# Kernel optimization log

Hardware: AMD Instinct MI355X
Metric: run time of the kernel (lower is better)

Reference implementation:

```python
import jax, jax.numpy as jnp
import numpy as np

N_NODES = 100000
N_EDGES = 1250000
D_FEAT = 64
K = 10          # propagation steps (hardcoded in module)
ALPHA = 0.1     # teleport probability (hardcoded in module)


def setup_inputs() -> dict:
    key = jax.random.key(0)
    k1, k2 = jax.random.split(key)
    x = jax.random.normal(k1, (N_NODES, D_FEAT), dtype=jnp.float32)
    # edge_index[0] = source nodes (j), edge_index[1] = target nodes (i)
    edge_index = jax.random.randint(k2, (2, N_EDGES), 0, N_NODES, dtype=jnp.int32)
    return {"x": x, "edge_index": edge_index}


def reference(x, edge_index):
    # PyG APPNP with add_self_loops=False, dropout=0:
    #   gcn_norm: deg[i] = sum of unit edge weights into i (scatter on col)
    #   norm_e = deg^{-1/2}[row_e] * deg^{-1/2}[col_e]
    #   h_{k+1} = (1 - alpha) * A_hat h_k + alpha * x
    row, col = edge_index[0], edge_index[1]
    ones = jnp.ones((edge_index.shape[1],), dtype=x.dtype)
    deg = jax.ops.segment_sum(ones, col, num_segments=N_NODES)
    dinv_sqrt = jnp.where(deg > 0, jax.lax.rsqrt(jnp.where(deg > 0, deg, 1.0)), 0.0)
    norm = dinv_sqrt[row] * dinv_sqrt[col]  # [E]

    h = x
    for _ in range(K):
        # gather-scale-scatter: messages norm_e * h[src_e], aggregated at dst_e
        msg = norm[:, None] * h[row]                           # [E, D]
        agg = jax.ops.segment_sum(msg, col, num_segments=N_NODES)  # [N, D]
        h = (1.0 - ALPHA) * agg + ALPHA * x
    return h
```

## Files before the change

### kernel.cpp

```cpp
#include <hip/hip_runtime.h>

constexpr int DFEAT  = 64;
constexpr int KSTEPS = 10;
constexpr float ALPHA = 0.1f;
constexpr int PAD    = 4;
constexpr int BSHIFT = 8;
constexpr int MAXBUCK = 512;
constexpr int GR_A   = 128;

constexpr int SCAN_T    = 256;
constexpr int SCAN_I    = 4;
constexpr int SCAN_TILE = SCAN_T * SCAN_I;

typedef unsigned int u32;
typedef __attribute__((ext_vector_type(4))) unsigned int u32x4;

__device__ inline u32 f2bf(float f) {
    u32 u = __float_as_uint(f);
    return ((u + 0x7fffu + ((u >> 16) & 1u)) >> 16) & 0xFFFFu;
}
__device__ inline float bfLO(u32 v) { return __uint_as_float(v << 16); }
__device__ inline float bfHI(u32 v) { return __uint_as_float(v & 0xFFFF0000u); }

__global__ void __launch_bounds__(256) k_hA(
    const int* __restrict__ col, int* __restrict__ blockhist,
    int E, int nb, int chunk) {
    __shared__ int hist[MAXBUCK];
    int t  = threadIdx.x;
    int e0 = blockIdx.x * chunk;
    int e1 = min(E, e0 + chunk);
    for (int b = t; b < MAXBUCK; b += 256) hist[b] = 0;
    __syncthreads();
    for (int e = e0 + t; e < e1; e += 256)
        atomicAdd(&hist[col[e] >> BSHIFT], 1);
    __syncthreads();
    for (int b = t; b < nb; b += 256)
        blockhist[blockIdx.x * MAXBUCK + b] = hist[b];
}

__global__ void k_colsum(int* __restrict__ blockhist, int* __restrict__ btotal) {
    __shared__ int s[GR_A];
    int b = blockIdx.x, t = threadIdx.x;
    int v = blockhist[t * MAXBUCK + b];
    s[t] = v;
    __syncthreads();
    for (int o = 1; o < GR_A; o <<= 1) {
        int u = (t >= o) ? s[t - o] : 0;
        __syncthreads();
        s[t] += u;
        __syncthreads();
    }
    blockhist[t * MAXBUCK + b] = s[t] - v;
    if (t == GR_A - 1) btotal[b] = s[t];
}

__global__ void k_bscan(const int* __restrict__ btotal, int* __restrict__ bstart,
                        int nb) {
    __shared__ int s[MAXBUCK];
    int t = threadIdx.x;
    if (t < nb) s[t] = btotal[t];
    __syncthreads();
    if (t == 0) {
        int acc = 0;
        for (int i = 0; i < nb; ++i) { int v = s[i]; s[i] = acc; acc += v; }
    }
    __syncthreads();
    if (t < nb) bstart[t] = s[t];
}

__global__ void __launch_bounds__(256) k_hB(
    const int* __restrict__ row, const int* __restrict__ col,
    const int* __restrict__ blockhist, const int* __restrict__ bstart,
    u32* __restrict__ bucketed, int E, int nb, int chunk) {
    __shared__ int cur[MAXBUCK];
    int t  = threadIdx.x;
    int e0 = blockIdx.x * chunk;
    int e1 = min(E, e0 + chunk);
    for (int b = t; b < nb; b += 256)
        cur[b] = bstart[b] + blockhist[blockIdx.x * MAXBUCK + b];
    __syncthreads();
    for (int e = e0 + t; e < e1; e += 256) {
        int c = col[e], r = row[e];
        int rank = atomicAdd(&cur[c >> BSHIFT], 1);
        bucketed[rank] = ((u32)r << BSHIFT) | (u32)(c & ((1 << BSHIFT) - 1));
    }
}

__global__ void __launch_bounds__(256) k_degB(
    const u32* __restrict__ bucketed, const int* __restrict__ bstart,
    const int* __restrict__ btotal, float* __restrict__ dinv,
    int* __restrict__ dpad, int N) {
    __shared__ int cnt[256];
    int b = blockIdx.x, t = threadIdx.x;
    cnt[t] = 0;
    __syncthreads();
    int p0 = bstart[b], p1 = p0 + btotal[b];
    for (int p = p0 + t; p < p1; p += 256)
        atomicAdd(&cnt[bucketed[p] & 255u], 1);
    __syncthreads();
    int node = (b << BSHIFT) + t;
    if (node < N) {
        int d = cnt[t];
        dinv[node] = (d > 0) ? rsqrtf((float)d) : 0.0f;
        dpad[node] = (d + (PAD - 1)) & ~(PAD - 1);
    }
}

__global__ void k_scan1(const int* __restrict__ in, int* __restrict__ out,
                        int* __restrict__ bsum, int n) {
    __shared__ int s[SCAN_T];
    int tid  = threadIdx.x;
    int base = blockIdx.x * SCAN_TILE + tid * SCAN_I;
    int v[SCAN_I];
    int sum = 0;
#pragma unroll
    for (int j = 0; j < SCAN_I; ++j) {
        v[j] = (base + j < n) ? in[base + j] : 0;
        sum += v[j];
    }
    s[tid] = sum;
    __syncthreads();
    for (int ofs = 1; ofs < SCAN_T; ofs <<= 1) {
        int t = (tid >= ofs) ? s[tid - ofs] : 0;
        __syncthreads();
        s[tid] += t;
        __syncthreads();
    }
    int excl = (tid == 0) ? 0 : s[tid - 1];
    if (tid == SCAN_T - 1) bsum[blockIdx.x] = s[tid];
#pragma unroll
    for (int j = 0; j < SCAN_I; ++j) {
        if (base + j < n) out[base + j] = excl;
        excl += v[j];
    }
}

__global__ void k_scan2(int* __restrict__ bsum, int nb) {
    if (threadIdx.x == 0 && blockIdx.x == 0) {
        int acc = 0;
        for (int i = 0; i < nb; ++i) { int t = bsum[i]; bsum[i] = acc; acc += t; }
    }
}

__global__ void k_scan3(int* __restrict__ offs, const int* __restrict__ bsum, int n) {
    int add  = bsum[blockIdx.x];
    int base = blockIdx.x * SCAN_TILE + threadIdx.x * SCAN_I;
#pragma unroll
    for (int j = 0; j < SCAN_I; ++j) {
        int i = base + j;
        if (i < n) offs[i] += add;
    }
}

__global__ void __launch_bounds__(256) k_fillB(
    const u32* __restrict__ bucketed, const int* __restrict__ bstart,
    const int* __restrict__ btotal, const int* __restrict__ offs,
    const float* __restrict__ dinv, u32* __restrict__ meta, int N) {
    __shared__ int   lcur[256];
    __shared__ float ldinv[256];
    int b = blockIdx.x, t = threadIdx.x;
    int node = (b << BSHIFT) + t;
    lcur[t]  = (node < N) ? offs[node] : 0;
    ldinv[t] = (node < N) ? dinv[node] : 0.0f;
    __syncthreads();
    int p0 = bstart[b], p1 = p0 + btotal[b];
    for (int p = p0 + t; p < p1; p += 256) {
        u32 v  = bucketed[p];
        int r  = (int)(v >> BSHIFT);
        int cl = (int)(v & 255u);
        int pos = atomicAdd(&lcur[cl], 1);
        float w = dinv[r] * ldinv[cl];
        u32 wq = (u32)__float2int_rn(w * 32768.0f);
        if (wq > 32767u) wq = 32767u;
        meta[pos] = (wq << 17) | (u32)r;
    }
}

__global__ void k_cvt(const float* __restrict__ x, u32* __restrict__ xb, int n8) {
    int stride = gridDim.x * blockDim.x;
    const float4* x4 = (const float4*)x;
    u32x4* o4 = (u32x4*)xb;
    for (int i = blockIdx.x * blockDim.x + threadIdx.x; i < n8; i += stride) {
        float4 a = x4[2 * i], b = x4[2 * i + 1];
        u32x4 o;
        o.x = (f2bf(a.y) << 16) | f2bf(a.x);
        o.y = (f2bf(a.w) << 16) | f2bf(a.z);
        o.z = (f2bf(b.y) << 16) | f2bf(b.x);
        o.w = (f2bf(b.w) << 16) | f2bf(b.z);
        o4[i] = o;
    }
}

template<bool LAST>
__global__ void __launch_bounds__(256) k_prop(
    const int* __restrict__ offs, const int* __restrict__ dpad,
    const u32* __restrict__ meta, const u32* __restrict__ hsrc,
    const float* __restrict__ x, const u32* __restrict__ xb,
    void* __restrict__ hdst, int N) {
    int gid = (int)((blockIdx.x * blockDim.x + threadIdx.x) >> 3);
    int l   = threadIdx.x & 7;
    if (gid >= N) return;
    int j   = offs[gid];
    int end = j + dpad[gid];

    const u32x4* h4 = (const u32x4*)hsrc;
    float a0 = 0.f, a1 = 0.f, a2 = 0.f, a3 = 0.f,
          a4 = 0.f, a5 = 0.f, a6 = 0.f, a7 = 0.f;

    if (j < end) {
        u32x4 mq = *(const u32x4*)&meta[j];
        while (j < end) {
            int jn = j + 4;
            u32x4 mqn = *(const u32x4*)&meta[jn];
            u32x4 q0 = h4[(size_t)(mq.x & 0x1FFFFu) * 8 + l];
            u32x4 q1 = h4[(size_t)(mq.y & 0x1FFFFu) * 8 + l];
            u32x4 q2 = h4[(size_t)(mq.z & 0x1FFFFu) * 8 + l];
            u32x4 q3 = h4[(size_t)(mq.w & 0x1FFFFu) * 8 + l];
            float w0 = (float)(mq.x >> 17) * (1.0f / 32768.0f);
            float w1 = (float)(mq.y >> 17) * (1.0f / 32768.0f);
            float w2 = (float)(mq.z >> 17) * (1.0f / 32768.0f);
            float w3 = (float)(mq.w >> 17) * (1.0f / 32768.0f);
            a0 += w0 * bfLO(q0.x); a1 += w0 * bfHI(q0.x);
            a2 += w0 * bfLO(q0.y); a3 += w0 * bfHI(q0.y);
            a4 += w0 * bfLO(q0.z); a5 += w0 * bfHI(q0.z);
            a6 += w0 * bfLO(q0.w); a7 += w0 * bfHI(q0.w);
            a0 += w1 * bfLO(q1.x); a1 += w1 * bfHI(q1.x);
            a2 += w1 * bfLO(q1.y); a3 += w1 * bfHI(q1.y);
            a4 += w1 * bfLO(q1.z); a5 += w1 * bfHI(q1.z);
            a6 += w1 * bfLO(q1.w); a7 += w1 * bfHI(q1.w);
            a0 += w2 * bfLO(q2.x); a1 += w2 * bfHI(q2.x);
            a2 += w2 * bfLO(q2.y); a3 += w2 * bfHI(q2.y);
            a4 += w2 * bfLO(q2.z); a5 += w2 * bfHI(q2.z);
            a6 += w2 * bfLO(q2.w); a7 += w2 * bfHI(q2.w);
            a0 += w3 * bfLO(q3.x); a1 += w3 * bfHI(q3.x);
            a2 += w3 * bfLO(q3.y); a3 += w3 * bfHI(q3.y);
            a4 += w3 * bfLO(q3.z); a5 += w3 * bfHI(q3.z);
            a6 += w3 * bfLO(q3.w); a7 += w3 * bfHI(q3.w);
            mq = mqn; j = jn;
        }
    }

    if (LAST) {
        size_t base = (size_t)gid * DFEAT + (size_t)l * 8;
        float4 xa = *(const float4*)&x[base];
        float4 xc = *(const float4*)&x[base + 4];
        float r0 = (1.0f - ALPHA) * a0 + ALPHA * xa.x;
        float r1 = (1.0f - ALPHA) * a1 + ALPHA * xa.y;
        float r2 = (1.0f - ALPHA) * a2 + ALPHA * xa.z;
        float r3 = (1.0f - ALPHA) * a3 + ALPHA * xa.w;
        float r4 = (1.0f - ALPHA) * a4 + ALPHA * xc.x;
        float r5 = (1.0f - ALPHA) * a5 + ALPHA * xc.y;
        float r6 = (1.0f - ALPHA) * a6 + ALPHA * xc.z;
        float r7 = (1.0f - ALPHA) * a7 + ALPHA * xc.w;
        float* o = (float*)hdst;
        *(float4*)&o[base]     = make_float4(r0, r1, r2, r3);
        *(float4*)&o[base + 4] = make_float4(r4, r5, r6, r7);
    } else {
        u32x4 t = ((const u32x4*)xb)[(size_t)gid * 8 + l];
        float r0 = (1.0f - ALPHA) * a0 + ALPHA * bfLO(t.x);
        float r1 = (1.0f - ALPHA) * a1 + ALPHA * bfHI(t.x);
        float r2 = (1.0f - ALPHA) * a2 + ALPHA * bfLO(t.y);
        float r3 = (1.0f - ALPHA) * a3 + ALPHA * bfHI(t.y);
        float r4 = (1.0f - ALPHA) * a4 + ALPHA * bfLO(t.z);
        float r5 = (1.0f - ALPHA) * a5 + ALPHA * bfHI(t.z);
        float r6 = (1.0f - ALPHA) * a6 + ALPHA * bfLO(t.w);
        float r7 = (1.0f - ALPHA) * a7 + ALPHA * bfHI(t.w);
        u32x4 o;
        o.x = (f2bf(r1) << 16) | f2bf(r0);
        o.y = (f2bf(r3) << 16) | f2bf(r2);
        o.z = (f2bf(r5) << 16) | f2bf(r4);
        o.w = (f2bf(r7) << 16) | f2bf(r6);
        ((u32x4*)hdst)[(size_t)gid * 8 + l] = o;
    }
}

extern "C" void kernel_launch(void* const* d_in, const int* in_sizes, int n_in,
                              void* d_out, int out_size, void* d_ws, size_t ws_size,
                              hipStream_t stream) {
    const float* x  = (const float*)d_in[0];
    const int*   ei = (const int*)d_in[1];
    const int N = in_sizes[0] / DFEAT;
    const int E = in_sizes[1] / 2;
    const int* row = ei;
    const int* col = ei + E;

    const int NBUCK = (N + ((1 << BSHIFT) - 1)) >> BSHIFT;

    char* ws = (char*)d_ws;
    auto align256 = [](size_t v) { return (v + 255) & ~(size_t)255; };
    size_t off = 0;
    int* dpad = (int*)(ws + off);       off += align256((size_t)N * 4);
    float* dinv = (float*)(ws + off);   off += align256((size_t)N * 4);
    int* offs = (int*)(ws + off);       off += align256((size_t)N * 4);
    int* bsum = (int*)(ws + off);       off += align256((size_t)4096);
    int* btotal = (int*)(ws + off);     off += align256((size_t)MAXBUCK * 4);
    int* bstart = (int*)(ws + off);     off += align256((size_t)MAXBUCK * 4);
    int* blockhist = (int*)(ws + off);  off += align256((size_t)GR_A * MAXBUCK * 4);
    u32* bucketed = (u32*)(ws + off);   off += align256((size_t)E * 4);
    size_t metaCap = (size_t)E + (size_t)(PAD - 1) * N + 16;
    u32* meta = (u32*)(ws + off);       off += align256(metaCap * 4);
    u32* xb = (u32*)(ws + off);         off += align256((size_t)N * 32 * 4);
    u32* hA = (u32*)(ws + off);         off += align256((size_t)N * 32 * 4);
    u32* hB = (u32*)(ws + off);         off += align256((size_t)N * 32 * 4);

    float* out = (float*)d_out;

    const int BLK = 256;
    const int nb    = (N + SCAN_TILE - 1) / SCAN_TILE;
    const int n8    = N * DFEAT / 8;
    const int gridC = (n8 + BLK - 1) / BLK;
    const int gridProp = (N * 8 + BLK - 1) / BLK;
    const int chunkA = (E + GR_A - 1) / GR_A;

    hipMemsetAsync(meta, 0, metaCap * 4, stream);
    k_hA    <<<GR_A, BLK, 0, stream>>>(col, blockhist, E, NBUCK, chunkA);
    k_colsum<<<NBUCK, GR_A, 0, stream>>>(blockhist, btotal);
    k_bscan <<<1, MAXBUCK, 0, stream>>>(btotal, bstart, NBUCK);
    k_hB    <<<GR_A, BLK, 0, stream>>>(row, col, blockhist, bstart, bucketed,
                                       E, NBUCK, chunkA);
    k_degB  <<<NBUCK, BLK, 0, stream>>>(bucketed, bstart, btotal, dinv, dpad, N);
    k_scan1 <<<nb, SCAN_T, 0, stream>>>(dpad, offs, bsum, N);
    k_scan2 <<<1, 64, 0, stream>>>(bsum, nb);
    k_scan3 <<<nb, SCAN_T, 0, stream>>>(offs, bsum, N);
    k_fillB <<<NBUCK, BLK, 0, stream>>>(bucketed, bstart, btotal, offs, dinv, meta, N);
    k_cvt   <<<gridC, BLK, 0, stream>>>(x, xb, n8);

    u32* bufs[2] = { hA, hB };
    for (int k = 0; k < KSTEPS; ++k) {
        const u32* src = (k == 0) ? xb : bufs[(k + 1) & 1];
        if (k < KSTEPS - 1) {
            k_prop<false><<<gridProp, BLK, 0, stream>>>(offs, dpad, meta, src, x, xb,
                                                        (void*)bufs[k & 1], N);
        } else {
            k_prop<true><<<gridProp, BLK, 0, stream>>>(offs, dpad, meta, src, x, xb,
                                                       (void*)out, N);
        }
    }
    (void)ws_size; (void)n_in; (void)out_size;
}
```

Baseline: 340.7 us.

## Unroll propagation gather to 8 edges, fuse convert into histogram, drop scan2

Padding of each node's edge list rises from 4 to 8 so the propagation loop gathers eight neighbor rows per iteration, which raises memory-level parallelism. The cost is more zero-weight padded edges to load and process, since each node now pads to a multiple of 8. Separately, the bf16 conversion of x is merged into the histogram kernel by adding extra blocks, and the single-thread scan2 kernel is removed. In its place, each scan3 block serially sums the preceding block totals, which saves two kernel launches.

```diff
diff --git a/kernel.cpp b/kernel.cpp
--- a/kernel.cpp
+++ b/kernel.cpp
@@ -3,7 +3,7 @@
 constexpr int DFEAT  = 64;
 constexpr int KSTEPS = 10;
 constexpr float ALPHA = 0.1f;
-constexpr int PAD    = 4;
+constexpr int PAD    = 8;
 constexpr int BSHIFT = 8;
 constexpr int MAXBUCK = 512;
 constexpr int GR_A   = 128;
@@ -22,20 +22,36 @@
 __device__ inline float bfLO(u32 v) { return __uint_as_float(v << 16); }
 __device__ inline float bfHI(u32 v) { return __uint_as_float(v & 0xFFFF0000u); }
 
-__global__ void __launch_bounds__(256) k_hA(
+__global__ void __launch_bounds__(256) k_hA_cvt(
     const int* __restrict__ col, int* __restrict__ blockhist,
-    int E, int nb, int chunk) {
+    int E, int nb, int chunk,
+    const float* __restrict__ x, u32* __restrict__ xb, int n8) {
     __shared__ int hist[MAXBUCK];
-    int t  = threadIdx.x;
-    int e0 = blockIdx.x * chunk;
-    int e1 = min(E, e0 + chunk);
-    for (int b = t; b < MAXBUCK; b += 256) hist[b] = 0;
-    __syncthreads();
-    for (int e = e0 + t; e < e1; e += 256)
-        atomicAdd(&hist[col[e] >> BSHIFT], 1);
-    __syncthreads();
-    for (int b = t; b < nb; b += 256)
-        blockhist[blockIdx.x * MAXBUCK + b] = hist[b];
+    int t = threadIdx.x;
+    if ((int)blockIdx.x < GR_A) {
+        int e0 = blockIdx.x * chunk;
+        int e1 = min(E, e0 + chunk);
+        for (int b = t; b < MAXBUCK; b += 256) hist[b] = 0;
+        __syncthreads();
+        for (int e = e0 + t; e < e1; e += 256)
+            atomicAdd(&hist[col[e] >> BSHIFT], 1);
+        __syncthreads();
+        for (int b = t; b < nb; b += 256)
+            blockhist[blockIdx.x * MAXBUCK + b] = hist[b];
+    } else {
+        int stride = (gridDim.x - GR_A) * blockDim.x;
+        const float4* x4 = (const float4*)x;
+        u32x4* o4 = (u32x4*)xb;
+        for (int i = (blockIdx.x - GR_A) * blockDim.x + t; i < n8; i += stride) {
+            float4 a = x4[2 * i], b = x4[2 * i + 1];
+            u32x4 o;
+            o.x = (f2bf(a.y) << 16) | f2bf(a.x);
+            o.y = (f2bf(a.w) << 16) | f2bf(a.z);
+            o.z = (f2bf(b.y) << 16) | f2bf(b.x);
+            o.w = (f2bf(b.w) << 16) | f2bf(b.z);
+            o4[i] = o;
+        }
+    }
 }
 
 __global__ void k_colsum(int* __restrict__ blockhist, int* __restrict__ btotal) {
@@ -135,15 +151,15 @@
     }
 }
 
-__global__ void k_scan2(int* __restrict__ bsum, int nb) {
-    if (threadIdx.x == 0 && blockIdx.x == 0) {
+__global__ void k_scan3(int* __restrict__ offs, const int* __restrict__ bsum, int n) {
+    __shared__ int s_add;
+    if (threadIdx.x == 0) {
         int acc = 0;
-        for (int i = 0; i < nb; ++i) { int t = bsum[i]; bsum[i] = acc; acc += t; }
-    }
-}
-
-__global__ void k_scan3(int* __restrict__ offs, const int* __restrict__ bsum, int n) {
-    int add  = bsum[blockIdx.x];
+        for (int i = 0; i < (int)blockIdx.x; ++i) acc += bsum[i];
+        s_add = acc;
+    }
+    __syncthreads();
+    int add  = s_add;
     int base = blockIdx.x * SCAN_TILE + threadIdx.x * SCAN_I;
 #pragma unroll
     for (int j = 0; j < SCAN_I; ++j) {
@@ -173,21 +189,6 @@
         u32 wq = (u32)__float2int_rn(w * 32768.0f);
         if (wq > 32767u) wq = 32767u;
         meta[pos] = (wq << 17) | (u32)r;
-    }
-}
-
-__global__ void k_cvt(const float* __restrict__ x, u32* __restrict__ xb, int n8) {
-    int stride = gridDim.x * blockDim.x;
-    const float4* x4 = (const float4*)x;
-    u32x4* o4 = (u32x4*)xb;
-    for (int i = blockIdx.x * blockDim.x + threadIdx.x; i < n8; i += stride) {
-        float4 a = x4[2 * i], b = x4[2 * i + 1];
-        u32x4 o;
-        o.x = (f2bf(a.y) << 16) | f2bf(a.x);
-        o.y = (f2bf(a.w) << 16) | f2bf(a.z);
-        o.z = (f2bf(b.y) << 16) | f2bf(b.x);
-        o.w = (f2bf(b.w) << 16) | f2bf(b.z);
-        o4[i] = o;
     }
 }
 
@@ -208,18 +209,28 @@
           a4 = 0.f, a5 = 0.f, a6 = 0.f, a7 = 0.f;
 
     if (j < end) {
-        u32x4 mq = *(const u32x4*)&meta[j];
+        u32x4 mA = *(const u32x4*)&meta[j];
+        u32x4 mB = *(const u32x4*)&meta[j + 4];
         while (j < end) {
-            int jn = j + 4;
-            u32x4 mqn = *(const u32x4*)&meta[jn];
-            u32x4 q0 = h4[(size_t)(mq.x & 0x1FFFFu) * 8 + l];
-            u32x4 q1 = h4[(size_t)(mq.y & 0x1FFFFu) * 8 + l];
-            u32x4 q2 = h4[(size_t)(mq.z & 0x1FFFFu) * 8 + l];
-            u32x4 q3 = h4[(size_t)(mq.w & 0x1FFFFu) * 8 + l];
-            float w0 = (float)(mq.x >> 17) * (1.0f / 32768.0f);
-            float w1 = (float)(mq.y >> 17) * (1.0f / 32768.0f);
-            float w2 = (float)(mq.z >> 17) * (1.0f / 32768.0f);
-            float w3 = (float)(mq.w >> 17) * (1.0f / 32768.0f);
+            int jn = j + 8;
+            u32x4 q0 = h4[(size_t)(mA.x & 0x1FFFFu) * 8 + l];
+            u32x4 q1 = h4[(size_t)(mA.y & 0x1FFFFu) * 8 + l];
+            u32x4 q2 = h4[(size_t)(mA.z & 0x1FFFFu) * 8 + l];
+            u32x4 q3 = h4[(size_t)(mA.w & 0x1FFFFu) * 8 + l];
+            u32x4 q4 = h4[(size_t)(mB.x & 0x1FFFFu) * 8 + l];
+            u32x4 q5 = h4[(size_t)(mB.y & 0x1FFFFu) * 8 + l];
+            u32x4 q6 = h4[(size_t)(mB.z & 0x1FFFFu) * 8 + l];
+            u32x4 q7 = h4[(size_t)(mB.w & 0x1FFFFu) * 8 + l];
+            u32x4 mA2 = *(const u32x4*)&meta[jn];
+            u32x4 mB2 = *(const u32x4*)&meta[jn + 4];
+            float w0 = (float)(mA.x >> 17) * (1.0f / 32768.0f);
+            float w1 = (float)(mA.y >> 17) * (1.0f / 32768.0f);
+            float w2 = (float)(mA.z >> 17) * (1.0f / 32768.0f);
+            float w3 = (float)(mA.w >> 17) * (1.0f / 32768.0f);
+            float w4 = (float)(mB.x >> 17) * (1.0f / 32768.0f);
+            float w5 = (float)(mB.y >> 17) * (1.0f / 32768.0f);
+            float w6 = (float)(mB.z >> 17) * (1.0f / 32768.0f);
+            float w7 = (float)(mB.w >> 17) * (1.0f / 32768.0f);
             a0 += w0 * bfLO(q0.x); a1 += w0 * bfHI(q0.x);
             a2 += w0 * bfLO(q0.y); a3 += w0 * bfHI(q0.y);
             a4 += w0 * bfLO(q0.z); a5 += w0 * bfHI(q0.z);
@@ -236,7 +247,23 @@
             a2 += w3 * bfLO(q3.y); a3 += w3 * bfHI(q3.y);
             a4 += w3 * bfLO(q3.z); a5 += w3 * bfHI(q3.z);
             a6 += w3 * bfLO(q3.w); a7 += w3 * bfHI(q3.w);
-            mq = mqn; j = jn;
+            a0 += w4 * bfLO(q4.x); a1 += w4 * bfHI(q4.x);
+            a2 += w4 * bfLO(q4.y); a3 += w4 * bfHI(q4.y);
+            a4 += w4 * bfLO(q4.z); a5 += w4 * bfHI(q4.z);
+            a6 += w4 * bfLO(q4.w); a7 += w4 * bfHI(q4.w);
+            a0 += w5 * bfLO(q5.x); a1 += w5 * bfHI(q5.x);
+            a2 += w5 * bfLO(q5.y); a3 += w5 * bfHI(q5.y);
+            a4 += w5 * bfLO(q5.z); a5 += w5 * bfHI(q5.z);
+            a6 += w5 * bfLO(q5.w); a7 += w5 * bfHI(q5.w);
+            a0 += w6 * bfLO(q6.x); a1 += w6 * bfHI(q6.x);
+            a2 += w6 * bfLO(q6.y); a3 += w6 * bfHI(q6.y);
+            a4 += w6 * bfLO(q6.z); a5 += w6 * bfHI(q6.z);
+            a6 += w6 * bfLO(q6.w); a7 += w6 * bfHI(q6.w);
+            a0 += w7 * bfLO(q7.x); a1 += w7 * bfHI(q7.x);
+            a2 += w7 * bfLO(q7.y); a3 += w7 * bfHI(q7.y);
+            a4 += w7 * bfLO(q7.z); a5 += w7 * bfHI(q7.z);
+            a6 += w7 * bfLO(q7.w); a7 += w7 * bfHI(q7.w);
+            mA = mA2; mB = mB2; j = jn;
         }
     }
 
@@ -297,7 +324,7 @@
     int* bstart = (int*)(ws + off);     off += align256((size_t)MAXBUCK * 4);
     int* blockhist = (int*)(ws + off);  off += align256((size_t)GR_A * MAXBUCK * 4);
     u32* bucketed = (u32*)(ws + off);   off += align256((size_t)E * 4);
-    size_t metaCap = (size_t)E + (size_t)(PAD - 1) * N + 16;
+    size_t metaCap = (size_t)E + (size_t)(PAD - 1) * N + 32;
     u32* meta = (u32*)(ws + off);       off += align256(metaCap * 4);
     u32* xb = (u32*)(ws + off);         off += align256((size_t)N * 32 * 4);
     u32* hA = (u32*)(ws + off);         off += align256((size_t)N * 32 * 4);
@@ -313,17 +340,16 @@
     const int chunkA = (E + GR_A - 1) / GR_A;
 
     hipMemsetAsync(meta, 0, metaCap * 4, stream);
-    k_hA    <<<GR_A, BLK, 0, stream>>>(col, blockhist, E, NBUCK, chunkA);
+    k_hA_cvt<<<GR_A + gridC, BLK, 0, stream>>>(col, blockhist, E, NBUCK, chunkA,
+                                               x, xb, n8);
     k_colsum<<<NBUCK, GR_A, 0, stream>>>(blockhist, btotal);
     k_bscan <<<1, MAXBUCK, 0, stream>>>(btotal, bstart, NBUCK);
     k_hB    <<<GR_A, BLK, 0, stream>>>(row, col, blockhist, bstart, bucketed,
                                        E, NBUCK, chunkA);
     k_degB  <<<NBUCK, BLK, 0, stream>>>(bucketed, bstart, btotal, dinv, dpad, N);
     k_scan1 <<<nb, SCAN_T, 0, stream>>>(dpad, offs, bsum, N);
-    k_scan2 <<<1, 64, 0, stream>>>(bsum, nb);
     k_scan3 <<<nb, SCAN_T, 0, stream>>>(offs, bsum, N);
     k_fillB <<<NBUCK, BLK, 0, stream>>>(bucketed, bstart, btotal, offs, dinv, meta, N);
-    k_cvt   <<<gridC, BLK, 0, stream>>>(x, xb, n8);
 
     u32* bufs[2] = { hA, hB };
     for (int k = 0; k < KSTEPS; ++k) {
```

After: 334.1 us. About the same (-1.9%).
